# Performance work log

Hardware: AMD Instinct MI355X
Metric: run time of the kernel (lower is better)

The kernel has to match this reference:

```python
import jax, jax.numpy as jnp
import numpy as np
import itertools

N_INPUTS = 6
N_TERMS = 4
# static rule index table [R, n_inputs], R = n_terms ** n_inputs = 4096
RULE_IDX = np.array(list(itertools.product(range(N_TERMS), repeat=N_INPUTS)), dtype=np.int32)


def setup_inputs() -> dict:
    key = jax.random.key(0)
    k1, k2, k3, k4 = jax.random.split(key, 4)
    B = 32768
    x = jax.random.normal(k1, (B, N_INPUTS), dtype=jnp.float32)
    centers = jax.random.normal(k2, (N_INPUTS, N_TERMS), dtype=jnp.float32)
    sigmas = jax.random.uniform(k3, (N_INPUTS, N_TERMS), dtype=jnp.float32, minval=0.5, maxval=1.5)
    consequents = jax.random.normal(k4, (N_TERMS ** N_INPUTS, N_INPUTS + 1), dtype=jnp.float32)
    return {"x": x, "centers": centers, "sigmas": sigmas, "consequents": consequents}


def reference(x, centers, sigmas, consequents):
    # Gaussian memberships: mu[b, i, t]
    s = jnp.abs(sigmas) + 1e-6                          # [I, T]
    mu = jnp.exp(-((x[:, :, None] - centers[None]) ** 2) / (2.0 * s[None] ** 2))  # [B, I, T]
    # rule firing strengths: product over inputs of selected terms
    idx = jnp.asarray(RULE_IDX.T)                       # [I, R]
    mu_sel = jnp.take_along_axis(mu, idx[None], axis=2)  # [B, I, R]
    w = jnp.prod(mu_sel, axis=1)                        # [B, R]
    w_norm = w / (jnp.sum(w, axis=1, keepdims=True) + 1e-8)
    # consequent outputs: f[b, r] = [x, 1] @ consequents[r]
    x_aug = jnp.concatenate([x, jnp.ones((x.shape[0], 1), dtype=x.dtype)], axis=1)  # [B, I+1]
    f = x_aug @ consequents.T                           # [B, R]
    return jnp.sum(w_norm * f, axis=1, keepdims=True)   # [B, 1]
```

## Files before the change

kernel.cpp:

```cpp
#include <hip/hip_runtime.h>


typedef __attribute__((ext_vector_type(8))) short bf16x8;
typedef __attribute__((ext_vector_type(4))) float f32x4;

#define THREADS 256
#define TAB_STR 65
#define TAB_BYTES (64 * TAB_STR * 16)

__device__ __forceinline__ unsigned int bf16rne(float f) {
    unsigned int u = __float_as_uint(f);
    u += 0x7fffu + ((u >> 16) & 1u);
    return u >> 16;
}

__device__ __forceinline__ float sel4(float a0, float a1, float a2, float a3, int i) {
    float lo = (i & 1) ? a1 : a0;
    float hi = (i & 1) ? a3 : a2;
    return (i & 2) ? hi : lo;
}

extern __shared__ uint4 tab[];

__launch_bounds__(THREADS, 2)
__global__ void anfis_one(const float* __restrict__ x,
                          const float* __restrict__ centers,
                          const float* __restrict__ sigmas,
                          const float* __restrict__ cons,
                          float* __restrict__ out, int B) {
    __shared__ float4 xs4[96];
    float* xs = (float*)xs4;

    const int tid  = threadIdx.x;
    const int lane = tid & 63;
    const int wv   = tid >> 6;
    const long blockbase = (long)blockIdx.x * 64;

    if (lane < 24) {
        long i4 = (long)blockIdx.x * 96 + wv * 24 + lane;
        float4 v = (i4 * 4 + 3 < (long)B * 6) ? ((const float4*)x)[i4]
                                              : make_float4(0.f, 0.f, 0.f, 0.f);
        xs4[wv * 24 + lane] = v;
    }

#pragma unroll 4
    for (int i = 0; i < 16; ++i) {
        int n = wv + 4 * i;
        const float* src = cons + (n * 64 + lane) * 7;
        unsigned int h0 = bf16rne(src[0]), h1 = bf16rne(src[1]);
        unsigned int h2 = bf16rne(src[2]), h3 = bf16rne(src[3]);
        unsigned int h4 = bf16rne(src[4]), h5 = bf16rne(src[5]);
        unsigned int h6 = bf16rne(src[6]);
        uint4 v;
        v.x = h0 | (h1 << 16);
        v.y = h2 | (h3 << 16);
        v.z = h4 | (h5 << 16);
        v.w = h6;
        tab[lane * TAB_STR + n] = v;
    }

    const int t = lane & 15, q = lane >> 4;
    const int lmA = wv * 16 + t;

    float cenv[6][4], invv[6][4];
#pragma unroll
    for (int i = 0; i < 6; ++i)
#pragma unroll
        for (int tm = 0; tm < 4; ++tm) {
            cenv[i][tm] = centers[i * 4 + tm];
            float s = fabsf(sigmas[i * 4 + tm]) + 1e-6f;
            invv[i][tm] = 0.5f / (s * s);
        }

    float xA[6];
#pragma unroll
    for (int j = 0; j < 6; ++j) xA[j] = xs[lmA * 6 + j];

    float E[6][4];
#pragma unroll
    for (int i = 0; i < 6; ++i)
#pragma unroll
        for (int tm = 0; tm < 4; ++tm) {
            float d = xA[i] - cenv[i][tm];
            E[i][tm] = __expf(-d * d * invv[i][tm]);
        }
    float den_local = (E[0][0] + E[0][1] + E[0][2] + E[0][3])
                    * (E[1][0] + E[1][1] + E[1][2] + E[1][3])
                    * (E[2][0] + E[2][1] + E[2][2] + E[2][3])
                    * (E[3][0] + E[3][1] + E[3][2] + E[3][3])
                    * (E[4][0] + E[4][1] + E[4][2] + E[4][3])
                    * (E[5][0] + E[5][1] + E[5][2] + E[5][3]);

    float e5q = sel4(E[5][0], E[5][1], E[5][2], E[5][3], q);
    float pt16[16];
#pragma unroll
    for (int kt = 0; kt < 16; ++kt)
        pt16[kt] = E[3][kt >> 2] * E[4][kt & 3] * e5q;

    float PH16[4][4];
    {
        const int tm1 = t >> 2, tm2 = t & 3;
        float c1 = sel4(cenv[1][0], cenv[1][1], cenv[1][2], cenv[1][3], tm1);
        float i1 = sel4(invv[1][0], invv[1][1], invv[1][2], invv[1][3], tm1);
        float c2 = sel4(cenv[2][0], cenv[2][1], cenv[2][2], cenv[2][3], tm2);
        float i2 = sel4(invv[2][0], invv[2][1], invv[2][2], invv[2][3], tm2);
#pragma unroll
        for (int r = 0; r < 4; ++r) {
            int lr = wv * 16 + q * 4 + r;
            float x0 = xs[lr * 6 + 0];
            float x1 = xs[lr * 6 + 1];
            float x2 = xs[lr * 6 + 2];
            float d1 = x1 - c1, d2 = x2 - c2;
            float G12 = __expf(-d1 * d1 * i1) * __expf(-d2 * d2 * i2);
#pragma unroll
            for (int nt = 0; nt < 4; ++nt) {
                float d0 = x0 - cenv[0][nt];
                PH16[r][nt] = G12 * __expf(-d0 * d0 * invv[0][nt]);
            }
        }
    }

    float xa[8];
#pragma unroll
    for (int j = 0; j < 6; ++j) xa[j] = xA[j];
    xa[6] = 1.f;
    xa[7] = 0.f;

    __syncthreads();

    union U4 { unsigned int u[4]; bf16x8 v; };
    f32x4 Dn[4];
#pragma unroll
    for (int nt = 0; nt < 4; ++nt) Dn[nt] = (f32x4){0.f, 0.f, 0.f, 0.f};

#pragma unroll 4
    for (int kt = 0; kt < 16; ++kt) {
        const uint4* base = &tab[(kt * 4 + q) * TAB_STR + t];
        U4 Bf[4];
#pragma unroll
        for (int nt = 0; nt < 4; ++nt) {
            uint4 bw = base[nt * 16];
            Bf[nt].u[0] = bw.x; Bf[nt].u[1] = bw.y;
            Bf[nt].u[2] = bw.z; Bf[nt].u[3] = bw.w;
        }
        float ptv = pt16[kt];
        U4 Ah, Al;
#pragma unroll
        for (int jp = 0; jp < 4; ++jp) {
            float u0 = ptv * xa[2 * jp];
            float u1 = ptv * xa[2 * jp + 1];
            unsigned int b0 = __float_as_uint(u0), b1 = __float_as_uint(u1);
            unsigned int t0 = b0 & 0xffff0000u, t1 = b1 & 0xffff0000u;
            float l0 = u0 - __uint_as_float(t0);
            float l1 = u1 - __uint_as_float(t1);
            Ah.u[jp] = (b0 >> 16) | t1;
            Al.u[jp] = (__float_as_uint(l0) >> 16) | (__float_as_uint(l1) & 0xffff0000u);
        }
#pragma unroll
        for (int nt = 0; nt < 4; ++nt)
            Dn[nt] = __builtin_amdgcn_mfma_f32_16x16x32_bf16(Ah.v, Bf[nt].v, Dn[nt], 0, 0, 0);
#pragma unroll
        for (int nt = 0; nt < 4; ++nt)
            Dn[nt] = __builtin_amdgcn_mfma_f32_16x16x32_bf16(Al.v, Bf[nt].v, Dn[nt], 0, 0, 0);
    }

    float Pn[4] = {0.f, 0.f, 0.f, 0.f};
#pragma unroll
    for (int nt = 0; nt < 4; ++nt)
#pragma unroll
        for (int r = 0; r < 4; ++r)
            Pn[r] = fmaf(PH16[r][nt], Dn[nt][r], Pn[r]);
#pragma unroll
    for (int off = 1; off < 16; off <<= 1)
#pragma unroll
        for (int r = 0; r < 4; ++r)
            Pn[r] += __shfl_xor(Pn[r], off);

    float dq[4];
#pragma unroll
    for (int r = 0; r < 4; ++r)
        dq[r] = __shfl(den_local, q * 4 + r);

    if (t == 0) {
        long bo = blockbase + wv * 16 + q * 4;
        float o[4];
#pragma unroll
        for (int r = 0; r < 4; ++r) o[r] = Pn[r] / (dq[r] + 1e-8f);
        if (bo + 3 < B) {
            *(float4*)&out[bo] = make_float4(o[0], o[1], o[2], o[3]);
        } else {
#pragma unroll
            for (int r = 0; r < 4; ++r)
                if (bo + r < B) out[bo + r] = o[r];
        }
    }
}

extern "C" void kernel_launch(void* const* d_in, const int* in_sizes, int n_in,
                              void* d_out, int out_size, void* d_ws, size_t ws_size,
                              hipStream_t stream) {
    const float* x       = (const float*)d_in[0];
    const float* centers = (const float*)d_in[1];
    const float* sigmas  = (const float*)d_in[2];
    const float* cons    = (const float*)d_in[3];
    float* out = (float*)d_out;

    int B = in_sizes[0] / 6;
    hipFuncSetAttribute(reinterpret_cast<const void*>(anfis_one),
                        hipFuncAttributeMaxDynamicSharedMemorySize, TAB_BYTES);
    int blocks = (B + 63) / 64;
    anfis_one<<<blocks, THREADS, TAB_BYTES, stream>>>(x, centers, sigmas, cons,
                                                      out, B);
}
```

Before: 69.20 us.

## Switch MFMA to single-pass fp16, vectorize consequent table staging

Replaces the split hi/lo bf16 MFMA pair with a single fp16 MFMA per tile, which halves the matrix instructions and removes the bit-splitting arithmetic. Consequent loading into LDS now uses coalesced float4 reads with packed fp16 conversion instead of strided scalar loads with manual bf16 rounding. Accumulators are split across two alternating sets to shorten MFMA dependency chains. The cost is reduced precision: fp16 products and pkrtz truncation may lose accuracy or overflow, and more accumulator registers are used.

```diff
diff --git a/kernel.cpp b/kernel.cpp
--- a/kernel.cpp
+++ b/kernel.cpp
@@ -1,17 +1,17 @@
 #include <hip/hip_runtime.h>
 
 
-typedef __attribute__((ext_vector_type(8))) short bf16x8;
+typedef __attribute__((ext_vector_type(8))) _Float16 f16x8;
 typedef __attribute__((ext_vector_type(4))) float f32x4;
 
 #define THREADS 256
 #define TAB_STR 65
 #define TAB_BYTES (64 * TAB_STR * 16)
 
-__device__ __forceinline__ unsigned int bf16rne(float f) {
-    unsigned int u = __float_as_uint(f);
-    u += 0x7fffu + ((u >> 16) & 1u);
-    return u >> 16;
+__device__ __forceinline__ unsigned int pkh(float a, float b) {
+    union { __fp16 h __attribute__((ext_vector_type(2))); unsigned int u; } z;
+    z.h = __builtin_amdgcn_cvt_pkrtz(a, b);
+    return z.u;
 }
 
 __device__ __forceinline__ float sel4(float a0, float a1, float a2, float a3, int i) {
@@ -43,20 +43,27 @@
         xs4[wv * 24 + lane] = v;
     }
 
-#pragma unroll 4
-    for (int i = 0; i < 16; ++i) {
-        int n = wv + 4 * i;
-        const float* src = cons + (n * 64 + lane) * 7;
-        unsigned int h0 = bf16rne(src[0]), h1 = bf16rne(src[1]);
-        unsigned int h2 = bf16rne(src[2]), h3 = bf16rne(src[3]);
-        unsigned int h4 = bf16rne(src[4]), h5 = bf16rne(src[5]);
-        unsigned int h6 = bf16rne(src[6]);
-        uint4 v;
-        v.x = h0 | (h1 << 16);
-        v.y = h2 | (h3 << 16);
-        v.z = h4 | (h5 << 16);
-        v.w = h6;
-        tab[lane * TAB_STR + n] = v;
+    {
+        const float4* cons4 = (const float4*)cons;
+        const int base4 = tid * 28;
+        const int n     = tid >> 2;
+        const int lbase = (tid & 3) * 16;
+#pragma unroll
+        for (int i = 0; i < 4; ++i) {
+            float F[28];
+            float4* Fv = (float4*)F;
+#pragma unroll
+            for (int j = 0; j < 7; ++j) Fv[j] = cons4[base4 + i * 7 + j];
+#pragma unroll
+            for (int m = 0; m < 4; ++m) {
+                uint4 v;
+                v.x = pkh(F[m * 7 + 0], F[m * 7 + 1]);
+                v.y = pkh(F[m * 7 + 2], F[m * 7 + 3]);
+                v.z = pkh(F[m * 7 + 4], F[m * 7 + 5]);
+                v.w = pkh(F[m * 7 + 6], 0.f);
+                tab[(lbase + i * 4 + m) * TAB_STR + n] = v;
+            }
+        }
     }
 
     const int t = lane & 15, q = lane >> 4;
@@ -120,18 +127,16 @@
         }
     }
 
-    float xa[8];
+    float xa[6];
 #pragma unroll
     for (int j = 0; j < 6; ++j) xa[j] = xA[j];
-    xa[6] = 1.f;
-    xa[7] = 0.f;
 
     __syncthreads();
 
-    union U4 { unsigned int u[4]; bf16x8 v; };
-    f32x4 Dn[4];
-#pragma unroll
-    for (int nt = 0; nt < 4; ++nt) Dn[nt] = (f32x4){0.f, 0.f, 0.f, 0.f};
+    union U4 { unsigned int u[4]; f16x8 v; };
+    f32x4 Dn[8];
+#pragma unroll
+    for (int a = 0; a < 8; ++a) Dn[a] = (f32x4){0.f, 0.f, 0.f, 0.f};
 
 #pragma unroll 4
     for (int kt = 0; kt < 16; ++kt) {
@@ -144,24 +149,16 @@
             Bf[nt].u[2] = bw.z; Bf[nt].u[3] = bw.w;
         }
         float ptv = pt16[kt];
-        U4 Ah, Al;
-#pragma unroll
-        for (int jp = 0; jp < 4; ++jp) {
-            float u0 = ptv * xa[2 * jp];
-            float u1 = ptv * xa[2 * jp + 1];
-            unsigned int b0 = __float_as_uint(u0), b1 = __float_as_uint(u1);
-            unsigned int t0 = b0 & 0xffff0000u, t1 = b1 & 0xffff0000u;
-            float l0 = u0 - __uint_as_float(t0);
-            float l1 = u1 - __uint_as_float(t1);
-            Ah.u[jp] = (b0 >> 16) | t1;
-            Al.u[jp] = (__float_as_uint(l0) >> 16) | (__float_as_uint(l1) & 0xffff0000u);
-        }
+        U4 Af;
+        Af.u[0] = pkh(ptv * xa[0], ptv * xa[1]);
+        Af.u[1] = pkh(ptv * xa[2], ptv * xa[3]);
+        Af.u[2] = pkh(ptv * xa[4], ptv * xa[5]);
+        Af.u[3] = pkh(ptv, 0.f);
+        const int ab = (kt & 1) * 4;
 #pragma unroll
         for (int nt = 0; nt < 4; ++nt)
-            Dn[nt] = __builtin_amdgcn_mfma_f32_16x16x32_bf16(Ah.v, Bf[nt].v, Dn[nt], 0, 0, 0);
-#pragma unroll
-        for (int nt = 0; nt < 4; ++nt)
-            Dn[nt] = __builtin_amdgcn_mfma_f32_16x16x32_bf16(Al.v, Bf[nt].v, Dn[nt], 0, 0, 0);
+            Dn[ab + nt] = __builtin_amdgcn_mfma_f32_16x16x32_f16(
+                Af.v, Bf[nt].v, Dn[ab + nt], 0, 0, 0);
     }
 
     float Pn[4] = {0.f, 0.f, 0.f, 0.f};
@@ -169,7 +166,7 @@
     for (int nt = 0; nt < 4; ++nt)
 #pragma unroll
         for (int r = 0; r < 4; ++r)
-            Pn[r] = fmaf(PH16[r][nt], Dn[nt][r], Pn[r]);
+            Pn[r] = fmaf(PH16[r][nt], Dn[nt][r] + Dn[4 + nt][r], Pn[r]);
 #pragma unroll
     for (int off = 1; off < 16; off <<= 1)
 #pragma unroll
@@ -206,8 +203,9 @@
     float* out = (float*)d_out;
 
     int B = in_sizes[0] / 6;
-    hipFuncSetAttribute(reinterpret_cast<const void*>(anfis_one),
-                        hipFuncAttributeMaxDynamicSharedMemorySize, TAB_BYTES);
+    (void)hipFuncSetAttribute(reinterpret_cast<const void*>(anfis_one),
+                              hipFuncAttributeMaxDynamicSharedMemorySize,
+                              TAB_BYTES);
     int blocks = (B + 63) / 64;
     anfis_one<<<blocks, THREADS, TAB_BYTES, stream>>>(x, centers, sigmas, cons,
                                                       out, B);
```

Result: no change. 68.18 us (-1.5%).
